# Kernel tuning notes

Hardware: AMD Instinct MI355X
Metric: run time of the kernel (lower is better)

## Reference

```python
import jax, jax.numpy as jnp
import numpy as np

B, T, C = 4, 2048, 1024
H = 16
D = C // H  # 64


def setup_inputs() -> dict:
    key = jax.random.key(0)
    ks = jax.random.split(key, 5)
    scale = 0.02
    x = jax.random.normal(ks[0], (B, T, C), dtype=jnp.float32)
    # Linear weights stored in [in, out] layout (equivalent to torch W.T)
    W_qkv = jax.random.normal(ks[1], (C, 3 * C), dtype=jnp.float32) * scale
    b_qkv = jax.random.normal(ks[2], (3 * C,), dtype=jnp.float32) * scale
    W_out = jax.random.normal(ks[3], (C, C), dtype=jnp.float32) * scale
    b_out = jax.random.normal(ks[4], (C,), dtype=jnp.float32) * scale
    return {"x": x, "W_qkv": W_qkv, "b_qkv": b_qkv, "W_out": W_out, "b_out": b_out}


def reference(x, W_qkv, b_qkv, W_out, b_out):
    Bx, Tx, Cx = x.shape
    qkv = x @ W_qkv + b_qkv                      # [B,T,3C]
    qkv = qkv.reshape(Bx, Tx, 3, H, D)
    q = jnp.transpose(qkv[:, :, 0], (0, 2, 1, 3))  # [B,H,T,D]
    k = jnp.transpose(qkv[:, :, 1], (0, 2, 1, 3))
    v = jnp.transpose(qkv[:, :, 2], (0, 2, 1, 3))
    scores = jnp.einsum('bhqd,bhkd->bhqk', q, k) / jnp.sqrt(jnp.float32(D))
    causal = jnp.tril(jnp.ones((Tx, Tx), dtype=bool))  # keep lower triangle
    scores = jnp.where(causal, scores, jnp.float32(-jnp.inf))
    w = jax.nn.softmax(scores, axis=-1)           # dropout p=0.0 (eval)
    out = jnp.einsum('bhqk,bhkd->bhqd', w, v)     # [B,H,T,D]
    out = jnp.transpose(out, (0, 2, 1, 3)).reshape(Bx, Tx, Cx)
    return out @ W_out + b_out
```

## Files before the change

### kernel.cpp

```cpp
#include <hip/hip_runtime.h>

typedef _Float16 f16;
typedef _Float16 f16x4 __attribute__((ext_vector_type(4)));
typedef _Float16 f16x8 __attribute__((ext_vector_type(8)));
typedef float    f32x4 __attribute__((ext_vector_type(4)));

#define B_ 4
#define T_ 2048
#define C_ 1024
#define H_ 16
#define D_ 64

__device__ __forceinline__ void gload_lds16(const f16* g, f16* l) {
  __builtin_amdgcn_global_load_lds(
      (const __attribute__((address_space(1))) unsigned int*)g,
      (__attribute__((address_space(3))) unsigned int*)l, 16, 0, 0);
}

__global__ void cvt_kernel(const float* __restrict__ in, f16* __restrict__ out, int n4) {
  int i = blockIdx.x * blockDim.x + threadIdx.x;
  int stride = gridDim.x * blockDim.x;
  for (; i < n4; i += stride) {
    float4 v = ((const float4*)in)[i];
    f16x4 h = { (f16)v.x, (f16)v.y, (f16)v.z, (f16)v.w };
    ((f16x4*)out)[i] = h;
  }
}

__global__ void transpose_cvt_kernel(const float* __restrict__ W, f16* __restrict__ Wt,
                                     int K, int N) {
  __shared__ f16 tile[32][33];
  int bx = blockIdx.x, by = blockIdx.y;
  int tx = threadIdx.x & 31, ty = threadIdx.x >> 5;
  #pragma unroll
  for (int i = ty; i < 32; i += 8)
    tile[i][tx] = (f16)W[(size_t)(by * 32 + i) * N + bx * 32 + tx];
  __syncthreads();
  #pragma unroll
  for (int i = ty; i < 32; i += 8)
    Wt[(size_t)(bx * 32 + i) * K + by * 32 + tx] = tile[tx][i];
}

template <int EPI>
__global__ __launch_bounds__(256, 3)
void gemm_kernel(const f16* __restrict__ A, const f16* __restrict__ Bt,
                 const float* __restrict__ bias, float* __restrict__ outF,
                 f16* __restrict__ q, f16* __restrict__ kk, f16* __restrict__ vt,
                 int M, int N, int K) {
  __shared__ __align__(16) f16 As[3][128 * 32];
  __shared__ __align__(16) f16 Bs[3][128 * 32];
  const int nbn = N >> 7;
  const int bid = blockIdx.x;
  const int bm = bid / nbn, bn = bid % nbn;
  const int m0 = bm << 7, n0 = bn << 7;
  const int tid = threadIdx.x;
  const int lane = tid & 63, wid = tid >> 6;
  const int wr = wid >> 1, wc = wid & 1;

  f32x4 acc[4][4] = {};

  const int srow = lane >> 2;
  const int scol = (((lane & 3) ^ ((lane >> 2) & 3)) << 3);
  const f16* Abase = A + (size_t)(m0 + srow) * K + scol;
  const f16* Bbase = Bt + (size_t)(n0 + srow) * K + scol;

  auto stage = [&](int buf, int kt) {
    const int c0 = wid * 2;
    #pragma unroll
    for (int c = c0; c < c0 + 2; ++c) {
      gload_lds16(Abase + (size_t)c * 16 * K + kt * 32, &As[buf][c * 512]);
      gload_lds16(Bbase + (size_t)c * 16 * K + kt * 32, &Bs[buf][c * 512]);
    }
  };

  const int g = lane >> 4;
  const int rr = lane & 15;
  const int swz = (g ^ (rr & 3)) << 4;

  auto compute = [&](int buf) {
    f16x8 af[4], bf[4];
    #pragma unroll
    for (int t = 0; t < 4; ++t) {
      af[t] = *(const f16x8*)((const char*)&As[buf][0] + (wr * 64 + t * 16 + rr) * 64 + swz);
      bf[t] = *(const f16x8*)((const char*)&Bs[buf][0] + (wc * 64 + t * 16 + rr) * 64 + swz);
    }
    __builtin_amdgcn_s_setprio(1);
    #pragma unroll
    for (int i = 0; i < 4; ++i)
      #pragma unroll
      for (int j = 0; j < 4; ++j)
        acc[i][j] = __builtin_amdgcn_mfma_f32_16x16x32_f16(af[i], bf[j], acc[i][j], 0, 0, 0);
    __builtin_amdgcn_s_setprio(0);
  };

  const int nk = K >> 5;
  int bcur = 0, bnext = 1, bnn = 2;
  stage(0, 0);
  stage(1, 1);
  asm volatile("s_waitcnt vmcnt(4)" ::: "memory");
  __builtin_amdgcn_s_barrier();
  __builtin_amdgcn_sched_barrier(0);
  for (int t = 0; t < nk; ++t) {
    if (t + 2 < nk) stage(bnn, t + 2);
    compute(bcur);
    if (t + 1 < nk) {
      if (t + 2 < nk) asm volatile("s_waitcnt vmcnt(4)" ::: "memory");
      else            asm volatile("s_waitcnt vmcnt(0)" ::: "memory");
      __builtin_amdgcn_s_barrier();
      __builtin_amdgcn_sched_barrier(0);
    }
    const int tmp = bcur; bcur = bnext; bnext = bnn; bnn = tmp;
  }

  const int col = lane & 15;
  const int row4 = (lane >> 4) << 2;
  #pragma unroll
  for (int i = 0; i < 4; ++i) {
    #pragma unroll
    for (int j = 0; j < 4; ++j) {
      const int n = n0 + wc * 64 + j * 16 + col;
      const float bn_ = bias[n];
      #pragma unroll
      for (int r = 0; r < 4; ++r) {
        const int m = m0 + wr * 64 + i * 16 + row4 + r;
        const float v = acc[i][j][r] + bn_;
        if (EPI == 1) {
          outF[(size_t)m * N + n] = v;
        } else {
          const int which = n >> 10;
          const int cc = n & 1023;
          const int h = cc >> 6, d = cc & 63;
          const int b = m >> 11, t = m & 2047;
          const size_t bh = (size_t)b * 16 + h;
          const f16 hv = (f16)v;
          if (which == 0)      q [(bh * T_ + t) * D_ + d] = hv;
          else if (which == 1) kk[(bh * T_ + t) * D_ + d] = hv;
          else                 vt[(bh * D_ + d) * T_ + t] = hv;
        }
      }
    }
  }
}

__global__ __launch_bounds__(256, 2)
void attn_kernel(const f16* __restrict__ Q, const f16* __restrict__ Kg,
                 const f16* __restrict__ Vt, f16* __restrict__ Aout) {
  __shared__ __align__(16) f16 Ks[4][64 * 64];
  __shared__ __align__(16) f16 Vs[4][64 * 64];
  __shared__ __align__(16) f16 Pt[4][32 * 64];

  const int bid = blockIdx.x;
  const int wgid = (bid & 7) * 64 + (bid >> 3);
  const int bh = wgid >> 3;
  const int pr = wgid & 7;
  const int lane = threadIdx.x & 63, w = threadIdx.x >> 6;
  const int col = lane & 15;
  const int g = lane >> 4;
  const int ko = g << 3;

  const f16* Qp = Q + (size_t)bh * T_ * D_;
  const f16* Kp = Kg + (size_t)bh * T_ * D_;
  const f16* Vp = Vt + (size_t)bh * D_ * T_;

  const int sr = lane >> 3;
  const int sc = ((lane & 7) ^ (sr & 7)) << 3;

  auto stage = [&](int buf, int kb) {
    #pragma unroll
    for (int c2 = 0; c2 < 2; ++c2) {
      const int c = (w << 1) + c2;
      gload_lds16(Kp + (size_t)(kb + (c << 3) + sr) * D_ + sc, &Ks[buf][c * 512]);
      gload_lds16(Vp + (size_t)((c << 3) + sr) * T_ + kb + sc, &Vs[buf][c * 512]);
    }
  };
  auto ldsK = [&](int buf, int krow, int d0) -> f16x8 {
    const int off = krow * 128 + ((d0 << 1) ^ ((krow & 7) << 4));
    return *(const f16x8*)((const char*)&Ks[buf][0] + off);
  };
  auto ldsV = [&](int buf, int drow, int k0) -> f16x8 {
    const int off = drow * 128 + ((k0 << 1) ^ ((drow & 7) << 4));
    return *(const f16x8*)((const char*)&Vs[buf][0] + off);
  };

  char* PtW = (char*)&Pt[w][0];
  const int b = bh >> 4, hd = bh & 15;

  #pragma unroll 1
  for (int tt = 0; tt < 2; ++tt) {
    const int ti = tt ? (15 - pr) : pr;
    const int qrow0 = (ti << 7) + (w << 5);
    const int np = ti + 1;

    f16x8 qf[2][2];
    #pragma unroll
    for (int h = 0; h < 2; ++h)
      #pragma unroll
      for (int s = 0; s < 2; ++s) {
        f16x8 t = *(const f16x8*)&Qp[(size_t)(qrow0 + h * 16 + col) * D_ + s * 32 + ko];
        #pragma unroll
        for (int e = 0; e < 8; ++e) t[e] = t[e] * (f16)0.125f;
        qf[h][s] = t;
      }

    f32x4 o[2][4] = {};
    float m[2] = {-1e30f, -1e30f}, l[2] = {0.f, 0.f};

    auto COMPUTE = [&](int buf, int kb) {
      f32x4 sc2[2][4] = {};
      #pragma unroll
      for (int s = 0; s < 2; ++s)
        #pragma unroll
        for (int mt = 0; mt < 4; ++mt) {
          f16x8 kf = ldsK(buf, mt * 16 + col, s * 32 + ko);
          sc2[0][mt] = __builtin_amdgcn_mfma_f32_16x16x32_f16(kf, qf[0][s], sc2[0][mt], 0, 0, 0);
          sc2[1][mt] = __builtin_amdgcn_mfma_f32_16x16x32_f16(kf, qf[1][s], sc2[1][mt], 0, 0, 0);
        }

      if (kb + 63 > qrow0) {
        #pragma unroll
        for (int mt = 0; mt < 4; ++mt)
          #pragma unroll
          for (int r = 0; r < 4; ++r) {
            const int kv = kb + mt * 16 + (g << 2) + r;
            if (kv > qrow0 + col)      sc2[0][mt][r] = -1e30f;
            if (kv > qrow0 + 16 + col) sc2[1][mt][r] = -1e30f;
          }
      }

      float mx[2];
      #pragma unroll
      for (int h = 0; h < 2; ++h) {
        float v = fmaxf(fmaxf(fmaxf(sc2[h][0][0], sc2[h][0][1]), fmaxf(sc2[h][0][2], sc2[h][0][3])),
                        fmaxf(fmaxf(sc2[h][1][0], sc2[h][1][1]), fmaxf(sc2[h][1][2], sc2[h][1][3])));
        v = fmaxf(v, fmaxf(fmaxf(fmaxf(sc2[h][2][0], sc2[h][2][1]), fmaxf(sc2[h][2][2], sc2[h][2][3])),
                           fmaxf(fmaxf(sc2[h][3][0], sc2[h][3][1]), fmaxf(sc2[h][3][2], sc2[h][3][3]))));
        v = fmaxf(v, __shfl_xor(v, 16, 64));
        v = fmaxf(v, __shfl_xor(v, 32, 64));
        mx[h] = v;
      }

      if (!__all(fmaxf(mx[0] - m[0], mx[1] - m[1]) <= 8.f)) {
        #pragma unroll
        for (int h = 0; h < 2; ++h) {
          const float mnew = fmaxf(m[h], mx[h]);
          const float alpha = __expf(m[h] - mnew);
          m[h] = mnew;
          l[h] *= alpha;
          #pragma unroll
          for (int mt = 0; mt < 4; ++mt)
            #pragma unroll
            for (int r = 0; r < 4; ++r) o[h][mt][r] *= alpha;
        }
      }

      #pragma unroll
      for (int h = 0; h < 2; ++h) {
        float rs = 0.f;
        #pragma unroll
        for (int mt = 0; mt < 4; ++mt) {
          f16x4 ph;
          #pragma unroll
          for (int r = 0; r < 4; ++r) {
            const float p = __expf(sc2[h][mt][r] - m[h]);
            rs += p;
            ph[r] = (f16)p;
          }
          *(f16x4*)(PtW + (h * 16 + col) * 128 + (((mt << 5) + (g << 3)) ^ ((col & 7) << 4))) = ph;
        }
        rs += __shfl_xor(rs, 16, 64);
        rs += __shfl_xor(rs, 32, 64);
        l[h] += rs;
      }

      #pragma unroll
      for (int s = 0; s < 2; ++s) {
        const int pcb = ((s << 6) + (g << 4)) ^ ((col & 7) << 4);
        f16x8 pb0 = *(const f16x8*)(PtW + col * 128 + pcb);
        f16x8 pb1 = *(const f16x8*)(PtW + (16 + col) * 128 + pcb);
        #pragma unroll
        for (int mt = 0; mt < 4; ++mt) {
          f16x8 vf = ldsV(buf, mt * 16 + col, s * 32 + ko);
          o[0][mt] = __builtin_amdgcn_mfma_f32_16x16x32_f16(vf, pb0, o[0][mt], 0, 0, 0);
          o[1][mt] = __builtin_amdgcn_mfma_f32_16x16x32_f16(vf, pb1, o[1][mt], 0, 0, 0);
        }
      }
    };

    stage(0, 0);
    stage(1, 64);
    asm volatile("s_waitcnt vmcnt(0)" ::: "memory");
    __builtin_amdgcn_s_barrier();
    __builtin_amdgcn_sched_barrier(0);

    #pragma unroll 1
    for (int j = 0; j < np; ++j) {
      const int kb0 = j << 7;
      const int s0 = (j << 1) & 3, s1 = ((j << 1) + 1) & 3;
      if (j + 1 < np) {
        stage((s0 + 2) & 3, kb0 + 128);
        stage((s1 + 2) & 3, kb0 + 192);
      }
      COMPUTE(s0, kb0);
      if (kb0 + 64 <= qrow0 + 31) COMPUTE(s1, kb0 + 64);

      __builtin_amdgcn_sched_barrier(0);
      asm volatile("s_waitcnt vmcnt(0)" ::: "memory");
      __builtin_amdgcn_s_barrier();
      __builtin_amdgcn_sched_barrier(0);
    }

    #pragma unroll
    for (int h = 0; h < 2; ++h) {
      const float inv = 1.0f / l[h];
      const int t = qrow0 + h * 16 + col;
      const size_t rowoff = ((size_t)b * T_ + t) * C_ + (size_t)hd * D_;
      #pragma unroll
      for (int mt = 0; mt < 4; ++mt) {
        f16x4 ov;
        #pragma unroll
        for (int r = 0; r < 4; ++r) ov[r] = (f16)(o[h][mt][r] * inv);
        *(f16x4*)&Aout[rowoff + mt * 16 + (g << 2)] = ov;
      }
    }
    __builtin_amdgcn_s_barrier();
  }
}

extern "C" void kernel_launch(void* const* d_in, const int* in_sizes, int n_in,
                              void* d_out, int out_size, void* d_ws, size_t ws_size,
                              hipStream_t stream) {
  const float* x    = (const float*)d_in[0];
  const float* Wqkv = (const float*)d_in[1];
  const float* bqkv = (const float*)d_in[2];
  const float* Wout = (const float*)d_in[3];
  const float* bout = (const float*)d_in[4];
  float* out = (float*)d_out;

  char* ws = (char*)d_ws;
  f16* xb     = (f16*)ws;
  f16* Wqkv_t = (f16*)(ws + (16u << 20));
  f16* Wout_t = (f16*)(ws + (22u << 20));
  f16* Qb     = (f16*)(ws + (24u << 20));
  f16* Kb     = (f16*)(ws + (40u << 20));
  f16* Vtb    = (f16*)(ws + (56u << 20));

  cvt_kernel<<<2048, 256, 0, stream>>>(x, xb, (B_ * T_ * C_) / 4);
  dim3 g1(3072 / 32, 1024 / 32);
  transpose_cvt_kernel<<<g1, 256, 0, stream>>>(Wqkv, Wqkv_t, 1024, 3072);
  dim3 g2(1024 / 32, 1024 / 32);
  transpose_cvt_kernel<<<g2, 256, 0, stream>>>(Wout, Wout_t, 1024, 1024);

  gemm_kernel<0><<<64 * 24, 256, 0, stream>>>(xb, Wqkv_t, bqkv, nullptr,
                                              Qb, Kb, Vtb, 8192, 3072, 1024);
  attn_kernel<<<512, 256, 0, stream>>>(Qb, Kb, Vtb, xb );
  gemm_kernel<1><<<64 * 8, 256, 0, stream>>>(xb, Wout_t, bout, out,
                                             nullptr, nullptr, nullptr, 8192, 1024, 1024);
}
```

Before: 207.9 us.

## Process both paired query tiles in one KV sweep, use exp2, merge transposes

The attention kernel now handles its two causal-paired query tiles (pr and 15-pr) together in a single pass over K/V. Each staged K/V tile is loaded once and reused for both tiles, instead of being streamed twice in sequential loops. The softmax now folds log2(e) into the Q scale and uses exp2f, with the rescale threshold adjusted to match. The two weight-transpose launches are merged into one kernel. The cost is roughly double the register state (two sets of Q fragments and accumulators), which may lower occupancy or cause spills.

```diff
diff --git a/kernel.cpp b/kernel.cpp
--- a/kernel.cpp
+++ b/kernel.cpp
@@ -27,10 +27,14 @@
   }
 }
 
-__global__ void transpose_cvt_kernel(const float* __restrict__ W, f16* __restrict__ Wt,
-                                     int K, int N) {
+__global__ void transpose2_kernel(const float* __restrict__ Wqkv, f16* __restrict__ WqkvT,
+                                  const float* __restrict__ Wout, f16* __restrict__ WoutT) {
   __shared__ f16 tile[32][33];
+  const int K = 1024;
   int bx = blockIdx.x, by = blockIdx.y;
+  const float* W; f16* Wt; int N;
+  if (bx < 96) { W = Wqkv; Wt = WqkvT; N = 3072; }
+  else         { W = Wout; Wt = WoutT; N = 1024; bx -= 96; }
   int tx = threadIdx.x & 31, ty = threadIdx.x >> 5;
   #pragma unroll
   for (int i = ty; i < 32; i += 8)
@@ -185,144 +189,156 @@
   char* PtW = (char*)&Pt[w][0];
   const int b = bh >> 4, hd = bh & 15;
 
-  #pragma unroll 1
-  for (int tt = 0; tt < 2; ++tt) {
-    const int ti = tt ? (15 - pr) : pr;
-    const int qrow0 = (ti << 7) + (w << 5);
-    const int np = ti + 1;
-
-    f16x8 qf[2][2];
-    #pragma unroll
-    for (int h = 0; h < 2; ++h)
-      #pragma unroll
-      for (int s = 0; s < 2; ++s) {
-        f16x8 t = *(const f16x8*)&Qp[(size_t)(qrow0 + h * 16 + col) * D_ + s * 32 + ko];
+  const int qA = (pr << 7) + (w << 5);
+  const int qB = ((15 - pr) << 7) + (w << 5);
+  const int nkv = 32 - 2 * pr;
+  const int ni = nkv >> 1;
+
+  const f16 qsc = (f16)(0.125f * 1.44269504f);
+  f16x8 qfA[2][2], qfB[2][2];
+  #pragma unroll
+  for (int h = 0; h < 2; ++h)
+    #pragma unroll
+    for (int s = 0; s < 2; ++s) {
+      f16x8 ta = *(const f16x8*)&Qp[(size_t)(qA + h * 16 + col) * D_ + s * 32 + ko];
+      f16x8 tb = *(const f16x8*)&Qp[(size_t)(qB + h * 16 + col) * D_ + s * 32 + ko];
+      #pragma unroll
+      for (int e = 0; e < 8; ++e) { ta[e] = ta[e] * qsc; tb[e] = tb[e] * qsc; }
+      qfA[h][s] = ta; qfB[h][s] = tb;
+    }
+
+  f32x4 oA[2][4] = {}, oB[2][4] = {};
+  float mA[2] = {-1e30f, -1e30f}, lA[2] = {0.f, 0.f};
+  float mB[2] = {-1e30f, -1e30f}, lB[2] = {0.f, 0.f};
+
+  auto COMPUTE = [&](int buf, int kb, const f16x8 (&qf)[2][2], f32x4 (&o)[2][4],
+                     float (&m)[2], float (&l)[2], int qrow0) {
+    f32x4 sc2[2][4] = {};
+    #pragma unroll
+    for (int s = 0; s < 2; ++s)
+      #pragma unroll
+      for (int mt = 0; mt < 4; ++mt) {
+        f16x8 kf = ldsK(buf, mt * 16 + col, s * 32 + ko);
+        sc2[0][mt] = __builtin_amdgcn_mfma_f32_16x16x32_f16(kf, qf[0][s], sc2[0][mt], 0, 0, 0);
+        sc2[1][mt] = __builtin_amdgcn_mfma_f32_16x16x32_f16(kf, qf[1][s], sc2[1][mt], 0, 0, 0);
+      }
+
+    if (kb + 63 > qrow0) {
+      #pragma unroll
+      for (int mt = 0; mt < 4; ++mt)
         #pragma unroll
-        for (int e = 0; e < 8; ++e) t[e] = t[e] * (f16)0.125f;
-        qf[h][s] = t;
-      }
-
-    f32x4 o[2][4] = {};
-    float m[2] = {-1e30f, -1e30f}, l[2] = {0.f, 0.f};
-
-    auto COMPUTE = [&](int buf, int kb) {
-      f32x4 sc2[2][4] = {};
-      #pragma unroll
-      for (int s = 0; s < 2; ++s)
-        #pragma unroll
-        for (int mt = 0; mt < 4; ++mt) {
-          f16x8 kf = ldsK(buf, mt * 16 + col, s * 32 + ko);
-          sc2[0][mt] = __builtin_amdgcn_mfma_f32_16x16x32_f16(kf, qf[0][s], sc2[0][mt], 0, 0, 0);
-          sc2[1][mt] = __builtin_amdgcn_mfma_f32_16x16x32_f16(kf, qf[1][s], sc2[1][mt], 0, 0, 0);
+        for (int r = 0; r < 4; ++r) {
+          const int kv = kb + mt * 16 + (g << 2) + r;
+          if (kv > qrow0 + col)      sc2[0][mt][r] = -1e30f;
+          if (kv > qrow0 + 16 + col) sc2[1][mt][r] = -1e30f;
         }
-
-      if (kb + 63 > qrow0) {
+    }
+
+    float mx[2];
+    #pragma unroll
+    for (int h = 0; h < 2; ++h) {
+      float v = fmaxf(fmaxf(fmaxf(sc2[h][0][0], sc2[h][0][1]), fmaxf(sc2[h][0][2], sc2[h][0][3])),
+                      fmaxf(fmaxf(sc2[h][1][0], sc2[h][1][1]), fmaxf(sc2[h][1][2], sc2[h][1][3])));
+      v = fmaxf(v, fmaxf(fmaxf(fmaxf(sc2[h][2][0], sc2[h][2][1]), fmaxf(sc2[h][2][2], sc2[h][2][3])),
+                         fmaxf(fmaxf(sc2[h][3][0], sc2[h][3][1]), fmaxf(sc2[h][3][2], sc2[h][3][3]))));
+      v = fmaxf(v, __shfl_xor(v, 16, 64));
+      v = fmaxf(v, __shfl_xor(v, 32, 64));
+      mx[h] = v;
+    }
+
+    if (!__all(fmaxf(mx[0] - m[0], mx[1] - m[1]) <= 11.54f)) {
+      #pragma unroll
+      for (int h = 0; h < 2; ++h) {
+        const float mnew = fmaxf(m[h], mx[h]);
+        const float alpha = exp2f(m[h] - mnew);
+        m[h] = mnew;
+        l[h] *= alpha;
         #pragma unroll
         for (int mt = 0; mt < 4; ++mt)
           #pragma unroll
-          for (int r = 0; r < 4; ++r) {
-            const int kv = kb + mt * 16 + (g << 2) + r;
-            if (kv > qrow0 + col)      sc2[0][mt][r] = -1e30f;
-            if (kv > qrow0 + 16 + col) sc2[1][mt][r] = -1e30f;
-          }
-      }
-
-      float mx[2];
-      #pragma unroll
-      for (int h = 0; h < 2; ++h) {
-        float v = fmaxf(fmaxf(fmaxf(sc2[h][0][0], sc2[h][0][1]), fmaxf(sc2[h][0][2], sc2[h][0][3])),
-                        fmaxf(fmaxf(sc2[h][1][0], sc2[h][1][1]), fmaxf(sc2[h][1][2], sc2[h][1][3])));
-        v = fmaxf(v, fmaxf(fmaxf(fmaxf(sc2[h][2][0], sc2[h][2][1]), fmaxf(sc2[h][2][2], sc2[h][2][3])),
-                           fmaxf(fmaxf(sc2[h][3][0], sc2[h][3][1]), fmaxf(sc2[h][3][2], sc2[h][3][3]))));
-        v = fmaxf(v, __shfl_xor(v, 16, 64));
-        v = fmaxf(v, __shfl_xor(v, 32, 64));
-        mx[h] = v;
-      }
-
-      if (!__all(fmaxf(mx[0] - m[0], mx[1] - m[1]) <= 8.f)) {
+          for (int r = 0; r < 4; ++r) o[h][mt][r] *= alpha;
+      }
+    }
+
+    #pragma unroll
+    for (int h = 0; h < 2; ++h) {
+      float rs = 0.f;
+      #pragma unroll
+      for (int mt = 0; mt < 4; ++mt) {
+        f16x4 ph;
         #pragma unroll
-        for (int h = 0; h < 2; ++h) {
-          const float mnew = fmaxf(m[h], mx[h]);
-          const float alpha = __expf(m[h] - mnew);
-          m[h] = mnew;
-          l[h] *= alpha;
-          #pragma unroll
-          for (int mt = 0; mt < 4; ++mt)
-            #pragma unroll
-            for (int r = 0; r < 4; ++r) o[h][mt][r] *= alpha;
+        for (int r = 0; r < 4; ++r) {
+          const float p = exp2f(sc2[h][mt][r] - m[h]);
+          rs += p;
+          ph[r] = (f16)p;
         }
-      }
-
-      #pragma unroll
-      for (int h = 0; h < 2; ++h) {
-        float rs = 0.f;
-        #pragma unroll
-        for (int mt = 0; mt < 4; ++mt) {
-          f16x4 ph;
-          #pragma unroll
-          for (int r = 0; r < 4; ++r) {
-            const float p = __expf(sc2[h][mt][r] - m[h]);
-            rs += p;
-            ph[r] = (f16)p;
-          }
-          *(f16x4*)(PtW + (h * 16 + col) * 128 + (((mt << 5) + (g << 3)) ^ ((col & 7) << 4))) = ph;
-        }
-        rs += __shfl_xor(rs, 16, 64);
-        rs += __shfl_xor(rs, 32, 64);
-        l[h] += rs;
-      }
-
-      #pragma unroll
-      for (int s = 0; s < 2; ++s) {
-        const int pcb = ((s << 6) + (g << 4)) ^ ((col & 7) << 4);
-        f16x8 pb0 = *(const f16x8*)(PtW + col * 128 + pcb);
-        f16x8 pb1 = *(const f16x8*)(PtW + (16 + col) * 128 + pcb);
-        #pragma unroll
-        for (int mt = 0; mt < 4; ++mt) {
-          f16x8 vf = ldsV(buf, mt * 16 + col, s * 32 + ko);
-          o[0][mt] = __builtin_amdgcn_mfma_f32_16x16x32_f16(vf, pb0, o[0][mt], 0, 0, 0);
-          o[1][mt] = __builtin_amdgcn_mfma_f32_16x16x32_f16(vf, pb1, o[1][mt], 0, 0, 0);
-        }
-      }
-    };
-
-    stage(0, 0);
-    stage(1, 64);
+        *(f16x4*)(PtW + (h * 16 + col) * 128 + (((mt << 5) + (g << 3)) ^ ((col & 7) << 4))) = ph;
+      }
+      rs += __shfl_xor(rs, 16, 64);
+      rs += __shfl_xor(rs, 32, 64);
+      l[h] += rs;
+    }
+
+    #pragma unroll
+    for (int s = 0; s < 2; ++s) {
+      const int pcb = ((s << 6) + (g << 4)) ^ ((col & 7) << 4);
+      f16x8 pb0 = *(const f16x8*)(PtW + col * 128 + pcb);
+      f16x8 pb1 = *(const f16x8*)(PtW + (16 + col) * 128 + pcb);
+      #pragma unroll
+      for (int mt = 0; mt < 4; ++mt) {
+        f16x8 vf = ldsV(buf, mt * 16 + col, s * 32 + ko);
+        o[0][mt] = __builtin_amdgcn_mfma_f32_16x16x32_f16(vf, pb0, o[0][mt], 0, 0, 0);
+        o[1][mt] = __builtin_amdgcn_mfma_f32_16x16x32_f16(vf, pb1, o[1][mt], 0, 0, 0);
+      }
+    }
+  };
+
+  stage(0, 0);
+  stage(1, 64);
+  asm volatile("s_waitcnt vmcnt(0)" ::: "memory");
+  __builtin_amdgcn_s_barrier();
+  __builtin_amdgcn_sched_barrier(0);
+
+  #pragma unroll 1
+  for (int j = 0; j < ni; ++j) {
+    const int kb0 = j << 7;
+    const int s0 = (j << 1) & 3, s1 = ((j << 1) + 1) & 3;
+    if (j + 1 < ni) {
+      stage((s0 + 2) & 3, kb0 + 128);
+      stage((s1 + 2) & 3, kb0 + 192);
+    }
+    COMPUTE(s0, kb0, qfB, oB, mB, lB, qB);
+    if (kb0 + 64 <= qB + 31) COMPUTE(s1, kb0 + 64, qfB, oB, mB, lB, qB);
+    if (kb0 <= qA + 31) {
+      COMPUTE(s0, kb0, qfA, oA, mA, lA, qA);
+      if (kb0 + 64 <= qA + 31) COMPUTE(s1, kb0 + 64, qfA, oA, mA, lA, qA);
+    }
+
+    __builtin_amdgcn_sched_barrier(0);
     asm volatile("s_waitcnt vmcnt(0)" ::: "memory");
     __builtin_amdgcn_s_barrier();
     __builtin_amdgcn_sched_barrier(0);
-
-    #pragma unroll 1
-    for (int j = 0; j < np; ++j) {
-      const int kb0 = j << 7;
-      const int s0 = (j << 1) & 3, s1 = ((j << 1) + 1) & 3;
-      if (j + 1 < np) {
-        stage((s0 + 2) & 3, kb0 + 128);
-        stage((s1 + 2) & 3, kb0 + 192);
-      }
-      COMPUTE(s0, kb0);
-      if (kb0 + 64 <= qrow0 + 31) COMPUTE(s1, kb0 + 64);
-
-      __builtin_amdgcn_sched_barrier(0);
-      asm volatile("s_waitcnt vmcnt(0)" ::: "memory");
-      __builtin_amdgcn_s_barrier();
-      __builtin_amdgcn_sched_barrier(0);
-    }
-
-    #pragma unroll
-    for (int h = 0; h < 2; ++h) {
-      const float inv = 1.0f / l[h];
-      const int t = qrow0 + h * 16 + col;
-      const size_t rowoff = ((size_t)b * T_ + t) * C_ + (size_t)hd * D_;
-      #pragma unroll
-      for (int mt = 0; mt < 4; ++mt) {
-        f16x4 ov;
-        #pragma unroll
-        for (int r = 0; r < 4; ++r) ov[r] = (f16)(o[h][mt][r] * inv);
-        *(f16x4*)&Aout[rowoff + mt * 16 + (g << 2)] = ov;
-      }
-    }
-    __builtin_amdgcn_s_barrier();
+  }
+
+  #pragma unroll
+  for (int h = 0; h < 2; ++h) {
+    const float invA = 1.0f / lA[h];
+    const float invB = 1.0f / lB[h];
+    const int tAq = qA + h * 16 + col;
+    const int tBq = qB + h * 16 + col;
+    const size_t offA = ((size_t)b * T_ + tAq) * C_ + (size_t)hd * D_;
+    const size_t offB = ((size_t)b * T_ + tBq) * C_ + (size_t)hd * D_;
+    #pragma unroll
+    for (int mt = 0; mt < 4; ++mt) {
+      f16x4 va, vb;
+      #pragma unroll
+      for (int r = 0; r < 4; ++r) {
+        va[r] = (f16)(oA[h][mt][r] * invA);
+        vb[r] = (f16)(oB[h][mt][r] * invB);
+      }
+      *(f16x4*)&Aout[offA + mt * 16 + (g << 2)] = va;
+      *(f16x4*)&Aout[offB + mt * 16 + (g << 2)] = vb;
+    }
   }
 }
 
@@ -345,10 +361,8 @@
   f16* Vtb    = (f16*)(ws + (56u << 20));
 
   cvt_kernel<<<2048, 256, 0, stream>>>(x, xb, (B_ * T_ * C_) / 4);
-  dim3 g1(3072 / 32, 1024 / 32);
-  transpose_cvt_kernel<<<g1, 256, 0, stream>>>(Wqkv, Wqkv_t, 1024, 3072);
-  dim3 g2(1024 / 32, 1024 / 32);
-  transpose_cvt_kernel<<<g2, 256, 0, stream>>>(Wout, Wout_t, 1024, 1024);
+  dim3 gt(128, 32);
+  transpose2_kernel<<<gt, 256, 0, stream>>>(Wqkv, Wqkv_t, Wout, Wout_t);
 
   gemm_kernel<0><<<64 * 24, 256, 0, stream>>>(xb, Wqkv_t, bqkv, nullptr,
                                               Qb, Kb, Vtb, 8192, 3072, 1024);
```

After: 218.9 us. 5.3% more time.
